# Performance work log

Measured on AMD Instinct MI355X. Metric: run time of the kernel, lower is better.

The kernel has to match this reference:

```python
import jax, jax.numpy as jnp
import numpy as np

KERNEL_MUL = 2.0
KERNEL_NUM = 5


def _mmd(src, tar):
    """Multi-bandwidth Gaussian-kernel MMD, matching torch MMDLoss.mmd."""
    B = src.shape[0]
    total = jnp.concatenate([src, tar], axis=0)          # [2B, D]
    sq = jnp.sum(total * total, axis=1)                  # [2B]
    # ||a-b||^2 = ||a||^2 + ||b||^2 - 2 a.b  (GEMM form of the broadcast subtract)
    dist = sq[:, None] + sq[None, :] - 2.0 * (total @ total.T)  # [2B, 2B]
    n = 2 * B
    # torch uses L2_distance.data -> bandwidth is detached from the graph
    bandwidth = jax.lax.stop_gradient(jnp.sum(dist)) / (n * n - n)
    bandwidth = bandwidth / (KERNEL_MUL ** (KERNEL_NUM // 2))
    kernel = sum(jnp.exp(-dist / (bandwidth * KERNEL_MUL ** k)) for k in range(KERNEL_NUM))
    XX = kernel[:B, :B]
    YY = kernel[B:, B:]
    XY = kernel[:B, B:]
    YX = kernel[B:, :B]
    return jnp.mean(XX + YY - XY - YX)


def setup_inputs() -> dict:
    key = jax.random.key(0)
    k1, k2, k3 = jax.random.split(key, 3)
    B, IN, OUT, L = 4096, 512, 256, 2
    x = jax.random.normal(k1, (B, IN), dtype=jnp.float32)
    W_aux = jax.random.normal(k2, (L, IN), dtype=jnp.float32) * (1.0 / np.sqrt(IN))
    b_aux = jnp.zeros((L,), dtype=jnp.float32)
    W = jax.random.normal(k3, (L, OUT, IN), dtype=jnp.float32) * (1.0 / np.sqrt(IN))
    b = jnp.zeros((L, OUT), dtype=jnp.float32)
    return {"x": x, "W_aux": W_aux, "b_aux": b_aux, "W": W, "b": b}


def reference(x, W_aux, b_aux, W, b):
    L = W.shape[0]
    gates = jax.nn.softmax(x @ W_aux.T + b_aux, axis=-1)      # [B, L]
    outs = jnp.einsum('bi,loi->blo', x, W) + b                # [B, L, out]
    combine = jnp.einsum('bl,blo->bo', gates, outs)           # soft-gated combine
    loss = 0.0
    for i in range(L):
        for j in range(i + 1, L):
            loss = loss + _mmd(outs[:, i, :], outs[:, j, :])
    inter_mmd = loss * 2.0 / (L * L - L)
    return combine, -inter_mmd
```

## Files before the change

### kernel.cpp

```cpp
#include <hip/hip_runtime.h>
#include <stdint.h>
#include <math.h>

typedef __attribute__((ext_vector_type(8))) __bf16 bf16x8;
typedef __attribute__((ext_vector_type(4))) __bf16 bf16x4;
typedef __attribute__((ext_vector_type(4))) float f32x4;

__device__ __forceinline__ void gload_lds16(const __bf16* g, __bf16* l) {
  __builtin_amdgcn_global_load_lds(
      (const __attribute__((address_space(1))) unsigned int*)g,
      (__attribute__((address_space(3))) unsigned int*)l,
      16, 0, 0);
}

__global__ __launch_bounds__(256) void k_outs(const float* __restrict__ x,
                                              const float* __restrict__ W,
                                              const float* __restrict__ bias,
                                              __bf16* __restrict__ totalbf,
                                              float* __restrict__ colsum,
                                              float* __restrict__ scal,
                                              float* __restrict__ out) {
  __shared__ __bf16 As[64][64];
  __shared__ __bf16 Bs[64][64];
  const int bj = blockIdx.x;
  const int bi = blockIdx.y;
  const int t = threadIdx.x;
  if (bj == 0 && bi == 0) {
    colsum[t] = 0.f;
    if (t < 8) scal[t] = 0.f;
    if (t == 0) out[1048576] = 0.f;
  }
  const int wid = t >> 6, lane = t & 63;
  const int wr = wid >> 1, wc = wid & 1;
  const int n16 = lane & 15, q = lane >> 4;
  const int sx = (n16 & 7) << 3;
  const int erow = t >> 4;
  const int c4 = (t & 15) << 2;

  f32x4 acc[2][2];
  f32x4 zero = {0.f, 0.f, 0.f, 0.f};
  for (int i = 0; i < 2; ++i)
    for (int j = 0; j < 2; ++j) acc[i][j] = zero;

  const int arow0 = bi * 64, brow0 = bj * 64;

  float4 ra[4], rb[4];
#pragma unroll
  for (int p = 0; p < 4; ++p) {
    int row = p * 16 + erow;
    ra[p] = *(const float4*)(x + (size_t)(arow0 + row) * 512 + c4);
    rb[p] = *(const float4*)(W + (size_t)(brow0 + row) * 512 + c4);
  }

  for (int kc = 0; kc < 512; kc += 64) {
#pragma unroll
    for (int p = 0; p < 4; ++p) {
      int row = p * 16 + erow;
      int col = c4 ^ ((row & 7) << 3);
      float4 va = ra[p];
      bf16x4 ba = {(__bf16)va.x, (__bf16)va.y, (__bf16)va.z, (__bf16)va.w};
      *(bf16x4*)&As[row][col] = ba;
      float4 vb = rb[p];
      bf16x4 bb = {(__bf16)vb.x, (__bf16)vb.y, (__bf16)vb.z, (__bf16)vb.w};
      *(bf16x4*)&Bs[row][col] = bb;
    }
    __syncthreads();
    if (kc < 448) {
#pragma unroll
      for (int p = 0; p < 4; ++p) {
        int row = p * 16 + erow;
        ra[p] = *(const float4*)(x + (size_t)(arow0 + row) * 512 + kc + 64 + c4);
        rb[p] = *(const float4*)(W + (size_t)(brow0 + row) * 512 + kc + 64 + c4);
      }
    }
#pragma unroll
    for (int ks = 0; ks < 2; ++ks) {
      bf16x8 af[2], bfr[2];
#pragma unroll
      for (int f = 0; f < 2; ++f) {
        af[f]  = *(const bf16x8*)&As[wr * 32 + f * 16 + n16][(ks * 32 + q * 8) ^ sx];
        bfr[f] = *(const bf16x8*)&Bs[wc * 32 + f * 16 + n16][(ks * 32 + q * 8) ^ sx];
      }
      for (int fr = 0; fr < 2; ++fr)
        for (int fc = 0; fc < 2; ++fc)
          acc[fr][fc] = __builtin_amdgcn_mfma_f32_16x16x32_bf16(af[fr], bfr[fc], acc[fr][fc], 0, 0, 0);
    }
    __syncthreads();
  }

  for (int fc = 0; fc < 2; ++fc) {
    int n_g = bj * 64 + wc * 32 + fc * 16 + n16;
    float bv = bias[n_g];
    int l = n_g >> 8, o = n_g & 255;
    for (int fr = 0; fr < 2; ++fr) {
      for (int r = 0; r < 4; ++r) {
        int m_g = bi * 64 + wr * 32 + fr * 16 + q * 4 + r;
        float v = acc[fr][fc][r] + bv;
        totalbf[(size_t)(l * 4096 + m_g) * 256 + o] = (__bf16)v;
      }
    }
  }
}

__global__ __launch_bounds__(256) void k_sqc(const __bf16* __restrict__ tot,
                                             const float* __restrict__ x,
                                             const float* __restrict__ Waux,
                                             const float* __restrict__ baux,
                                             float* __restrict__ sq,
                                             float* __restrict__ colsum,
                                             float* __restrict__ scal,
                                             float* __restrict__ out) {
  __shared__ float lcol[4][256];
  __shared__ float wsq[4];
  __shared__ unsigned int isLast;
  const int t = threadIdx.x;
  const int wave = t >> 6, lane = t & 63;

  const float4* wa = (const float4*)(Waux);
  const float4* wb = (const float4*)(Waux + 512);
  float4 a0 = wa[lane * 2], a1 = wa[lane * 2 + 1];
  float4 b0 = wb[lane * 2], b1 = wb[lane * 2 + 1];
  const float bx0 = baux[0], bx1 = baux[1];
  float g0[8], g1[8];
#pragma unroll
  for (int it = 0; it < 8; ++it) {
    int m = blockIdx.x * 32 + wave * 8 + it;
    const float4* xr = (const float4*)(x + (size_t)m * 512);
    float4 x0 = xr[lane * 2], x1 = xr[lane * 2 + 1];
    float p0 = x0.x * a0.x + x0.y * a0.y + x0.z * a0.z + x0.w * a0.w
             + x1.x * a1.x + x1.y * a1.y + x1.z * a1.z + x1.w * a1.w;
    float p1 = x0.x * b0.x + x0.y * b0.y + x0.z * b0.z + x0.w * b0.w
             + x1.x * b1.x + x1.y * b1.y + x1.z * b1.z + x1.w * b1.w;
    for (int off = 32; off; off >>= 1) {
      p0 += __shfl_xor(p0, off, 64);
      p1 += __shfl_xor(p1, off, 64);
    }
    p0 += bx0; p1 += bx1;
    float mm = fmaxf(p0, p1);
    float e0 = __expf(p0 - mm), e1 = __expf(p1 - mm);
    float inv = 1.f / (e0 + e1);
    g0[it] = e0 * inv;
    g1[it] = e1 * inv;
  }

  float c0 = 0.f, c1 = 0.f, c2 = 0.f, c3 = 0.f;
  float bsq = 0.f;
#pragma unroll
  for (int it = 0; it < 8; ++it) {
    int m = blockIdx.x * 32 + wave * 8 + it;
    bf16x4 v0 = *(const bf16x4*)(tot + (size_t)m * 256 + lane * 4);
    bf16x4 v1 = *(const bf16x4*)(tot + (size_t)(4096 + m) * 256 + lane * 4);
    float f00 = v0[0], f01 = v0[1], f02 = v0[2], f03 = v0[3];
    float f10 = v1[0], f11 = v1[1], f12 = v1[2], f13 = v1[3];
    float s0 = f00 * f00 + f01 * f01 + f02 * f02 + f03 * f03;
    float s1 = f10 * f10 + f11 * f11 + f12 * f12 + f13 * f13;
    for (int off = 32; off; off >>= 1) {
      s0 += __shfl_down(s0, off, 64);
      s1 += __shfl_down(s1, off, 64);
    }
    if (lane == 0) { sq[m] = s0; sq[4096 + m] = s1; bsq += s0 + s1; }
    c0 += f00 + f10; c1 += f01 + f11; c2 += f02 + f12; c3 += f03 + f13;
    float4 r;
    r.x = g0[it] * f00 + g1[it] * f10;
    r.y = g0[it] * f01 + g1[it] * f11;
    r.z = g0[it] * f02 + g1[it] * f12;
    r.w = g0[it] * f03 + g1[it] * f13;
    *(float4*)(out + (size_t)m * 256 + lane * 4) = r;
  }
  lcol[wave][lane * 4 + 0] = c0;
  lcol[wave][lane * 4 + 1] = c1;
  lcol[wave][lane * 4 + 2] = c2;
  lcol[wave][lane * 4 + 3] = c3;
  if (lane == 0) wsq[wave] = bsq;
  __syncthreads();
  float s2 = lcol[0][t] + lcol[1][t] + lcol[2][t] + lcol[3][t];
  atomicAdd(&colsum[t], s2);
  if (t == 0) atomicAdd(&scal[4], wsq[0] + wsq[1] + wsq[2] + wsq[3]);
  __threadfence();
  if (t == 0) {
    unsigned int c = atomicAdd((unsigned int*)(scal + 5), 1u);
    isLast = (c == 127u) ? 1u : 0u;
  }
  __syncthreads();
  if (isLast) {
    __threadfence();
    float cv = atomicAdd(&colsum[t], 0.0f);
    lcol[0][t] = cv * cv;
    __syncthreads();
    for (int off = 128; off; off >>= 1) {
      if (t < off) lcol[0][t] += lcol[0][t + off];
      __syncthreads();
    }
    if (t == 0) {
      float sumsq = atomicAdd(&scal[4], 0.0f);
      double sumdist = 2.0 * 8192.0 * (double)sumsq - 2.0 * (double)lcol[0][0];
      double bw = sumdist / (8192.0 * 8192.0 - 8192.0) / 4.0;
      scal[1] = (float)(1.4426950408889634 / (bw * 16.0));
      scal[2] = (float)bw;
    }
  }
}

__global__ __launch_bounds__(256) void k_gram(const __bf16* __restrict__ tot,
                                              const float* __restrict__ sq,
                                              const float* __restrict__ scal,
                                              float* __restrict__ out) {
  const int b = blockIdx.x;
  const int nid = (b & 7) * 260 + (b >> 3);
  int ti = (int)((129.0 - sqrt(129.0 * 129.0 - 8.0 * (double)nid)) * 0.5);
  while (64 * ti - ti * (ti - 1) / 2 > nid) --ti;
  while (64 * (ti + 1) - (ti + 1) * ti / 2 <= nid) ++ti;
  const int tj = ti + (nid - (64 * ti - ti * (ti - 1) / 2));

  __shared__ __bf16 As[2][128][64];
  __shared__ __bf16 Bs[2][128][64];
  __shared__ float sqi[128], sqj[128];
  __shared__ float wred[4];
  const int t = threadIdx.x;
  const int wid = t >> 6, lane = t & 63;
  const int wr = wid >> 1, wc = wid & 1;
  const int n16 = lane & 15, q = lane >> 4;
  const int sx = (n16 & 7) << 3;
  const int lr = lane >> 3;
  const int ls = lane & 7;

  const float g = scal[1];
  if (t < 128) sqi[t] = sq[ti * 128 + t] * g;
  else         sqj[t - 128] = sq[tj * 128 + (t - 128)] * g;

  f32x4 acc[4][4];
  f32x4 zero = {0.f, 0.f, 0.f, 0.f};
  for (int i = 0; i < 4; ++i)
    for (int j = 0; j < 4; ++j) acc[i][j] = zero;

  const __bf16* gA = tot + (size_t)(ti * 128 + wid * 32 + lr) * 256 + ((ls ^ lr) << 3);
  const __bf16* gB = tot + (size_t)(tj * 128 + wid * 32 + lr) * 256 + ((ls ^ lr) << 3);

#pragma unroll
  for (int p = 0; p < 4; ++p) {
    gload_lds16(gA + p * 8 * 256, &As[0][wid * 32 + p * 8][0]);
    gload_lds16(gB + p * 8 * 256, &Bs[0][wid * 32 + p * 8][0]);
  }
  __syncthreads();

  int buf = 0;
  for (int it = 0; it < 4; ++it) {
    if (it < 3) {
      const int kc = (it + 1) * 64;
#pragma unroll
      for (int p = 0; p < 4; ++p) {
        gload_lds16(gA + p * 8 * 256 + kc, &As[buf ^ 1][wid * 32 + p * 8][0]);
        gload_lds16(gB + p * 8 * 256 + kc, &Bs[buf ^ 1][wid * 32 + p * 8][0]);
      }
    }
#pragma unroll
    for (int ks = 0; ks < 2; ++ks) {
      bf16x8 af[4], bfr[4];
#pragma unroll
      for (int f = 0; f < 4; ++f) {
        af[f]  = *(const bf16x8*)&As[buf][wr * 64 + f * 16 + n16][(ks * 32 + q * 8) ^ sx];
        bfr[f] = *(const bf16x8*)&Bs[buf][wc * 64 + f * 16 + n16][(ks * 32 + q * 8) ^ sx];
      }
      for (int fr = 0; fr < 4; ++fr)
        for (int fc = 0; fc < 4; ++fc)
          acc[fr][fc] = __builtin_amdgcn_mfma_f32_16x16x32_bf16(af[fr], bfr[fc], acc[fr][fc], 0, 0, 0);
    }
    __syncthreads();
    buf ^= 1;
  }

  const float twog = 2.f * g;
  float lsum = 0.f;
  for (int fr = 0; fr < 4; ++fr) {
    for (int r = 0; r < 4; ++r) {
      float gsi = sqi[wr * 64 + fr * 16 + q * 4 + r];
      for (int fc = 0; fc < 4; ++fc) {
        float gsj = sqj[wc * 64 + fc * 16 + n16];
        float u = exp2f(fmaf(twog, acc[fr][fc][r], -(gsi + gsj)));
        float u2 = u * u, u4 = u2 * u2, u8 = u4 * u4;
        float s1 = fmaf(u8, u8, u8);
        lsum += (u + u2) + (u4 + s1);
      }
    }
  }
  for (int off = 32; off; off >>= 1) lsum += __shfl_down(lsum, off, 64);
  if (lane == 0) wred[wid] = lsum;
  __syncthreads();
  if (t == 0) {
    float blocksum = wred[0] + wred[1] + wred[2] + wred[3];
    float sgn = ((ti < 32) == (tj < 32)) ? 1.f : -1.f;
    float wgt = (ti == tj) ? sgn : 2.f * sgn;
    atomicAdd(out + 1048576, wgt * blocksum * (-1.f / 16777216.f));
  }
}

extern "C" void kernel_launch(void* const* d_in, const int* in_sizes, int n_in,
                              void* d_out, int out_size, void* d_ws, size_t ws_size,
                              hipStream_t stream) {
  const float* x    = (const float*)d_in[0];
  const float* Waux = (const float*)d_in[1];
  const float* baux = (const float*)d_in[2];
  const float* W    = (const float*)d_in[3];
  const float* bias = (const float*)d_in[4];
  float* out = (float*)d_out;

  char* ws = (char*)d_ws;
  __bf16* totalbf = (__bf16*)ws;
  float* sq      = (float*)(ws + 4194304);
  float* colsum  = (float*)(ws + 4227072);
  float* scal    = (float*)(ws + 4228096);

  k_outs<<<dim3(8, 64), 256, 0, stream>>>(x, W, bias, totalbf, colsum, scal, out);
  k_sqc<<<128, 256, 0, stream>>>(totalbf, x, Waux, baux, sq, colsum, scal, out);
  k_gram<<<2080, 256, 0, stream>>>(totalbf, sq, scal, out);
}
```

Before: 141.8 us.

## Double-buffer k_outs with direct global-to-LDS fp32 loads and widen k_sqc grid

The projection GEMM kernel now stages fp32 tiles of x and W straight into double-buffered LDS with global_load_lds, using an XOR swizzle. The fp32-to-bf16 conversion moves to fragment-read time. This is meant to overlap the next tile's load with the current MFMA work and drop the register round-trip, at the cost of four times more LDS (64 KB) and repeated conversions. Separately, k_sqc runs on 256 blocks of 16 rows instead of 128 blocks of 32, with the last-block counter updated to match.

Result: slower. 151.0 us (+6.5%).

```diff
diff --git a/kernel.cpp b/kernel.cpp
--- a/kernel.cpp
+++ b/kernel.cpp
@@ -7,6 +7,12 @@
 typedef __attribute__((ext_vector_type(4))) float f32x4;
 
 __device__ __forceinline__ void gload_lds16(const __bf16* g, __bf16* l) {
+  __builtin_amdgcn_global_load_lds(
+      (const __attribute__((address_space(1))) unsigned int*)g,
+      (__attribute__((address_space(3))) unsigned int*)l,
+      16, 0, 0);
+}
+__device__ __forceinline__ void gload_lds16f(const float* g, float* l) {
   __builtin_amdgcn_global_load_lds(
       (const __attribute__((address_space(1))) unsigned int*)g,
       (__attribute__((address_space(3))) unsigned int*)l,
@@ -20,8 +26,8 @@
                                               float* __restrict__ colsum,
                                               float* __restrict__ scal,
                                               float* __restrict__ out) {
-  __shared__ __bf16 As[64][64];
-  __shared__ __bf16 Bs[64][64];
+  __shared__ float As[2][64][64];
+  __shared__ float Bs[2][64][64];
   const int bj = blockIdx.x;
   const int bi = blockIdx.y;
   const int t = threadIdx.x;
@@ -33,9 +39,8 @@
   const int wid = t >> 6, lane = t & 63;
   const int wr = wid >> 1, wc = wid & 1;
   const int n16 = lane & 15, q = lane >> 4;
-  const int sx = (n16 & 7) << 3;
-  const int erow = t >> 4;
-  const int c4 = (t & 15) << 2;
+  const int lr = lane >> 4;
+  const int ls = lane & 15;
 
   f32x4 acc[2][2];
   f32x4 zero = {0.f, 0.f, 0.f, 0.f};
@@ -44,49 +49,47 @@
 
   const int arow0 = bi * 64, brow0 = bj * 64;
 
-  float4 ra[4], rb[4];
-#pragma unroll
-  for (int p = 0; p < 4; ++p) {
-    int row = p * 16 + erow;
-    ra[p] = *(const float4*)(x + (size_t)(arow0 + row) * 512 + c4);
-    rb[p] = *(const float4*)(W + (size_t)(brow0 + row) * 512 + c4);
-  }
-
-  for (int kc = 0; kc < 512; kc += 64) {
-#pragma unroll
-    for (int p = 0; p < 4; ++p) {
-      int row = p * 16 + erow;
-      int col = c4 ^ ((row & 7) << 3);
-      float4 va = ra[p];
-      bf16x4 ba = {(__bf16)va.x, (__bf16)va.y, (__bf16)va.z, (__bf16)va.w};
-      *(bf16x4*)&As[row][col] = ba;
-      float4 vb = rb[p];
-      bf16x4 bb = {(__bf16)vb.x, (__bf16)vb.y, (__bf16)vb.z, (__bf16)vb.w};
-      *(bf16x4*)&Bs[row][col] = bb;
-    }
-    __syncthreads();
-    if (kc < 448) {
-#pragma unroll
-      for (int p = 0; p < 4; ++p) {
-        int row = p * 16 + erow;
-        ra[p] = *(const float4*)(x + (size_t)(arow0 + row) * 512 + kc + 64 + c4);
-        rb[p] = *(const float4*)(W + (size_t)(brow0 + row) * 512 + kc + 64 + c4);
-      }
-    }
+#define STAGE_OUTS(B, KC)                                                      \
+  _Pragma("unroll") for (int p = 0; p < 4; ++p) {                              \
+    int rrel = p * 4 + lr;      \
+    int rw = wid * 16 + rrel;                                                  \
+    gload_lds16f(x + (size_t)(arow0 + rw) * 512 + (KC) + ((ls ^ rrel) << 2),   \
+                 &As[B][wid * 16 + p * 4][0]);                                 \
+    gload_lds16f(W + (size_t)(brow0 + rw) * 512 + (KC) + ((ls ^ rrel) << 2),   \
+                 &Bs[B][wid * 16 + p * 4][0]);                                 \
+  }
+
+  STAGE_OUTS(0, 0)
+  __syncthreads();
+
+  int buf = 0;
+  for (int it = 0; it < 8; ++it) {
+    if (it < 7) { STAGE_OUTS(buf ^ 1, (it + 1) * 64) }
 #pragma unroll
     for (int ks = 0; ks < 2; ++ks) {
       bf16x8 af[2], bfr[2];
 #pragma unroll
       for (int f = 0; f < 2; ++f) {
-        af[f]  = *(const bf16x8*)&As[wr * 32 + f * 16 + n16][(ks * 32 + q * 8) ^ sx];
-        bfr[f] = *(const bf16x8*)&Bs[wc * 32 + f * 16 + n16][(ks * 32 + q * 8) ^ sx];
+        int rowA = wr * 32 + f * 16 + n16;
+        int rowB = wc * 32 + f * 16 + n16;
+        int s0 = ks * 8 + q * 2;
+        f32x4 alo = *(const f32x4*)&As[buf][rowA][(s0 ^ n16) << 2];
+        f32x4 ahi = *(const f32x4*)&As[buf][rowA][((s0 + 1) ^ n16) << 2];
+        f32x4 blo = *(const f32x4*)&Bs[buf][rowB][(s0 ^ n16) << 2];
+        f32x4 bhi = *(const f32x4*)&Bs[buf][rowB][((s0 + 1) ^ n16) << 2];
+        af[f]  = (bf16x8){(__bf16)alo[0], (__bf16)alo[1], (__bf16)alo[2], (__bf16)alo[3],
+                          (__bf16)ahi[0], (__bf16)ahi[1], (__bf16)ahi[2], (__bf16)ahi[3]};
+        bfr[f] = (bf16x8){(__bf16)blo[0], (__bf16)blo[1], (__bf16)blo[2], (__bf16)blo[3],
+                          (__bf16)bhi[0], (__bf16)bhi[1], (__bf16)bhi[2], (__bf16)bhi[3]};
       }
       for (int fr = 0; fr < 2; ++fr)
         for (int fc = 0; fc < 2; ++fc)
           acc[fr][fc] = __builtin_amdgcn_mfma_f32_16x16x32_bf16(af[fr], bfr[fc], acc[fr][fc], 0, 0, 0);
     }
     __syncthreads();
-  }
+    buf ^= 1;
+  }
+#undef STAGE_OUTS
 
   for (int fc = 0; fc < 2; ++fc) {
     int n_g = bj * 64 + wc * 32 + fc * 16 + n16;
@@ -121,10 +124,10 @@
   float4 a0 = wa[lane * 2], a1 = wa[lane * 2 + 1];
   float4 b0 = wb[lane * 2], b1 = wb[lane * 2 + 1];
   const float bx0 = baux[0], bx1 = baux[1];
-  float g0[8], g1[8];
-#pragma unroll
-  for (int it = 0; it < 8; ++it) {
-    int m = blockIdx.x * 32 + wave * 8 + it;
+  float g0[4], g1[4];
+#pragma unroll
+  for (int it = 0; it < 4; ++it) {
+    int m = blockIdx.x * 16 + wave * 4 + it;
     const float4* xr = (const float4*)(x + (size_t)m * 512);
     float4 x0 = xr[lane * 2], x1 = xr[lane * 2 + 1];
     float p0 = x0.x * a0.x + x0.y * a0.y + x0.z * a0.z + x0.w * a0.w
@@ -146,8 +149,8 @@
   float c0 = 0.f, c1 = 0.f, c2 = 0.f, c3 = 0.f;
   float bsq = 0.f;
 #pragma unroll
-  for (int it = 0; it < 8; ++it) {
-    int m = blockIdx.x * 32 + wave * 8 + it;
+  for (int it = 0; it < 4; ++it) {
+    int m = blockIdx.x * 16 + wave * 4 + it;
     bf16x4 v0 = *(const bf16x4*)(tot + (size_t)m * 256 + lane * 4);
     bf16x4 v1 = *(const bf16x4*)(tot + (size_t)(4096 + m) * 256 + lane * 4);
     float f00 = v0[0], f01 = v0[1], f02 = v0[2], f03 = v0[3];
@@ -179,7 +182,7 @@
   __threadfence();
   if (t == 0) {
     unsigned int c = atomicAdd((unsigned int*)(scal + 5), 1u);
-    isLast = (c == 127u) ? 1u : 0u;
+    isLast = (c == 255u) ? 1u : 0u;
   }
   __syncthreads();
   if (isLast) {
@@ -311,6 +314,6 @@
   float* scal    = (float*)(ws + 4228096);
 
   k_outs<<<dim3(8, 64), 256, 0, stream>>>(x, W, bias, totalbf, colsum, scal, out);
-  k_sqc<<<128, 256, 0, stream>>>(totalbf, x, Waux, baux, sq, colsum, scal, out);
+  k_sqc<<<256, 256, 0, stream>>>(totalbf, x, Waux, baux, sq, colsum, scal, out);
   k_gram<<<2080, 256, 0, stream>>>(totalbf, sq, scal, out);
 }
```

## Store bf16 outputs in MFMA fragment-tiled layout and load Gram operands directly

Applied to the files above, without the earlier changes.

The intermediate bf16 activation buffer is written in a tiled layout that matches the 16x16x32 MFMA operand fragments. The Gram kernel then loads its A and B fragments straight from global memory into registers with contiguous 16-byte per-lane loads, removing the LDS double-buffered staging and its barriers. This cuts LDS traffic and synchronisation, but each wave now reloads fragments from global/L2 with no sharing between waves through LDS, so data reuse inside a block depends on the caches.

New measurement: 140.7 us. Within noise of the previous version (-0.8%).

```diff
diff --git a/kernel.cpp b/kernel.cpp
--- a/kernel.cpp
+++ b/kernel.cpp
@@ -6,11 +6,9 @@
 typedef __attribute__((ext_vector_type(4))) __bf16 bf16x4;
 typedef __attribute__((ext_vector_type(4))) float f32x4;
 
-__device__ __forceinline__ void gload_lds16(const __bf16* g, __bf16* l) {
-  __builtin_amdgcn_global_load_lds(
-      (const __attribute__((address_space(1))) unsigned int*)g,
-      (__attribute__((address_space(3))) unsigned int*)l,
-      16, 0, 0);
+__device__ __forceinline__ size_t tbidx(int row, int o) {
+  return ((size_t)(row >> 4) << 12) + ((o >> 5) << 9) +
+         (((o >> 3) & 3) << 7) + ((row & 15) << 3) + (o & 7);
 }
 
 __global__ __launch_bounds__(256) void k_outs(const float* __restrict__ x,
@@ -96,7 +94,7 @@
       for (int r = 0; r < 4; ++r) {
         int m_g = bi * 64 + wr * 32 + fr * 16 + q * 4 + r;
         float v = acc[fr][fc][r] + bv;
-        totalbf[(size_t)(l * 4096 + m_g) * 256 + o] = (__bf16)v;
+        totalbf[tbidx(l * 4096 + m_g, o)] = (__bf16)v;
       }
     }
   }
@@ -148,8 +146,8 @@
 #pragma unroll
   for (int it = 0; it < 8; ++it) {
     int m = blockIdx.x * 32 + wave * 8 + it;
-    bf16x4 v0 = *(const bf16x4*)(tot + (size_t)m * 256 + lane * 4);
-    bf16x4 v1 = *(const bf16x4*)(tot + (size_t)(4096 + m) * 256 + lane * 4);
+    bf16x4 v0 = *(const bf16x4*)(tot + tbidx(m, lane * 4));
+    bf16x4 v1 = *(const bf16x4*)(tot + tbidx(4096 + m, lane * 4));
     float f00 = v0[0], f01 = v0[1], f02 = v0[2], f03 = v0[3];
     float f10 = v1[0], f11 = v1[1], f12 = v1[2], f13 = v1[3];
     float s0 = f00 * f00 + f01 * f01 + f02 * f02 + f03 * f03;
@@ -212,17 +210,12 @@
   while (64 * (ti + 1) - (ti + 1) * ti / 2 <= nid) ++ti;
   const int tj = ti + (nid - (64 * ti - ti * (ti - 1) / 2));
 
-  __shared__ __bf16 As[2][128][64];
-  __shared__ __bf16 Bs[2][128][64];
   __shared__ float sqi[128], sqj[128];
   __shared__ float wred[4];
   const int t = threadIdx.x;
   const int wid = t >> 6, lane = t & 63;
   const int wr = wid >> 1, wc = wid & 1;
   const int n16 = lane & 15, q = lane >> 4;
-  const int sx = (n16 & 7) << 3;
-  const int lr = lane >> 3;
-  const int ls = lane & 7;
 
   const float g = scal[1];
   if (t < 128) sqi[t] = sq[ti * 128 + t] * g;
@@ -233,41 +226,23 @@
   for (int i = 0; i < 4; ++i)
     for (int j = 0; j < 4; ++j) acc[i][j] = zero;
 
-  const __bf16* gA = tot + (size_t)(ti * 128 + wid * 32 + lr) * 256 + ((ls ^ lr) << 3);
-  const __bf16* gB = tot + (size_t)(tj * 128 + wid * 32 + lr) * 256 + ((ls ^ lr) << 3);
-
-#pragma unroll
-  for (int p = 0; p < 4; ++p) {
-    gload_lds16(gA + p * 8 * 256, &As[0][wid * 32 + p * 8][0]);
-    gload_lds16(gB + p * 8 * 256, &Bs[0][wid * 32 + p * 8][0]);
-  }
-  __syncthreads();
-
-  int buf = 0;
-  for (int it = 0; it < 4; ++it) {
-    if (it < 3) {
-      const int kc = (it + 1) * 64;
-#pragma unroll
-      for (int p = 0; p < 4; ++p) {
-        gload_lds16(gA + p * 8 * 256 + kc, &As[buf ^ 1][wid * 32 + p * 8][0]);
-        gload_lds16(gB + p * 8 * 256 + kc, &Bs[buf ^ 1][wid * 32 + p * 8][0]);
-      }
-    }
-#pragma unroll
-    for (int ks = 0; ks < 2; ++ks) {
-      bf16x8 af[4], bfr[4];
-#pragma unroll
-      for (int f = 0; f < 4; ++f) {
-        af[f]  = *(const bf16x8*)&As[buf][wr * 64 + f * 16 + n16][(ks * 32 + q * 8) ^ sx];
-        bfr[f] = *(const bf16x8*)&Bs[buf][wc * 64 + f * 16 + n16][(ks * 32 + q * 8) ^ sx];
-      }
-      for (int fr = 0; fr < 4; ++fr)
-        for (int fc = 0; fc < 4; ++fc)
-          acc[fr][fc] = __builtin_amdgcn_mfma_f32_16x16x32_bf16(af[fr], bfr[fc], acc[fr][fc], 0, 0, 0);
-    }
-    __syncthreads();
-    buf ^= 1;
-  }
+  const __bf16* pA = tot + ((size_t)(ti * 8 + wr * 4) << 12) + lane * 8;
+  const __bf16* pB = tot + ((size_t)(tj * 8 + wc * 4) << 12) + lane * 8;
+
+#pragma unroll
+  for (int ks = 0; ks < 8; ++ks) {
+    bf16x8 af[4], bfr[4];
+#pragma unroll
+    for (int f = 0; f < 4; ++f) {
+      af[f]  = *(const bf16x8*)(pA + ((size_t)f << 12) + ((size_t)ks << 9));
+      bfr[f] = *(const bf16x8*)(pB + ((size_t)f << 12) + ((size_t)ks << 9));
+    }
+    for (int fr = 0; fr < 4; ++fr)
+      for (int fc = 0; fc < 4; ++fc)
+        acc[fr][fc] = __builtin_amdgcn_mfma_f32_16x16x32_bf16(af[fr], bfr[fc], acc[fr][fc], 0, 0, 0);
+  }
+
+  __syncthreads();
 
   const float twog = 2.f * g;
   float lsum = 0.f;
```
